# Kernel optimization log

Measured on AMD Instinct MI355X. Metric: run time of the kernel, lower is better.

Reference implementation:

```python
import jax, jax.numpy as jnp
import numpy as np
from jax import lax

EPS = 1e-5
NBITS_W = 4
NBITS_A = 4
HIDDEN = 192


def _ste(x, q):
    # straight-through estimator: forward q, backward identity
    return x + lax.stop_gradient(q - x)


def act_q(x, bit, signed):
    # ACT_Q: per-tensor uniform activation quantization with max-abs scale (STE)
    if bit >= 32:
        return x
    n = float(2 ** (bit - 1) - 1) if signed else float(2 ** bit - 1)
    scale = lax.stop_gradient(jnp.max(jnp.abs(x)) + 1e-8)
    lo = -1.0 if signed else 0.0
    xc = jnp.clip(x / scale, lo, 1.0)
    q = jnp.round(xc * n) / n * scale
    return _ste(x, q)


def weight_q(w, bit):
    # Conv2d_quan_cim weight quant: symmetric per-tensor max-abs uniform quant (STE)
    if bit >= 32:
        return w
    n = float(2 ** (bit - 1) - 1)
    scale = lax.stop_gradient(jnp.max(jnp.abs(w)) + 1e-8)
    q = jnp.round(jnp.clip(w / scale, -1.0, 1.0) * n) / n * scale
    return _ste(w, q)


def bn(x, g, b, m, v):
    # eval-mode BatchNorm2d over NCHW
    inv = lax.rsqrt(v + EPS)
    return (x - m[None, :, None, None]) * (g * inv)[None, :, None, None] + b[None, :, None, None]


def conv(x, w, stride=1, groups=1, pad=0):
    return lax.conv_general_dilated(
        x, w, (stride, stride), ((pad, pad), (pad, pad)),
        dimension_numbers=("NCHW", "OIHW", "NCHW"), feature_group_count=groups)


def setup_inputs() -> dict:
    key = jax.random.key(0)
    ks = jax.random.split(key, 16)
    f32 = jnp.float32
    return {
        "x": jax.random.normal(ks[0], (32, 32, 112, 112), dtype=f32),
        "w1": jax.random.normal(ks[1], (HIDDEN, 32, 1, 1), dtype=f32),
        "bn1_g": jax.random.uniform(ks[2], (HIDDEN,), dtype=f32),
        "bn1_b": jax.random.normal(ks[3], (HIDDEN,), dtype=f32),
        "bn1_m": jax.random.normal(ks[4], (HIDDEN,), dtype=f32),
        "bn1_v": jax.random.uniform(ks[5], (HIDDEN,), dtype=f32),
        "w_dw": jax.random.normal(ks[6], (HIDDEN, 1, 3, 3), dtype=f32),
        "bn2_g": jax.random.uniform(ks[7], (HIDDEN,), dtype=f32),
        "bn2_b": jax.random.normal(ks[8], (HIDDEN,), dtype=f32),
        "bn2_m": jax.random.normal(ks[9], (HIDDEN,), dtype=f32),
        "bn2_v": jax.random.uniform(ks[10], (HIDDEN,), dtype=f32),
        "w2": jax.random.normal(ks[11], (32, HIDDEN, 1, 1), dtype=f32),
        "bn3_g": jax.random.uniform(ks[12], (32,), dtype=f32),
        "bn3_b": jax.random.normal(ks[13], (32,), dtype=f32),
        "bn3_m": jax.random.normal(ks[14], (32,), dtype=f32),
        "bn3_v": jax.random.uniform(ks[15], (32,), dtype=f32),
    }


def reference(x, w1, bn1_g, bn1_b, bn1_m, bn1_v, w_dw, bn2_g, bn2_b, bn2_m, bn2_v,
              w2, bn3_g, bn3_b, bn3_m, bn3_v):
    # leading signed ACT_Q (first=False)
    h = act_q(x, NBITS_A, signed=True)
    # expand 1x1: Conv2d_quan_cim -> BN -> ReLU6 -> ACT_Q
    h = conv(h, weight_q(w1, NBITS_W))
    h = jnp.clip(bn(h, bn1_g, bn1_b, bn1_m, bn1_v), 0.0, 6.0)
    h = act_q(h, NBITS_A, signed=False)
    # depthwise 3x3: Conv2d_quan_cim_dw -> BN -> ReLU6 -> ACT_Q
    h = conv(h, weight_q(w_dw, NBITS_W), stride=1, groups=HIDDEN, pad=1)
    h = jnp.clip(bn(h, bn2_g, bn2_b, bn2_m, bn2_v), 0.0, 6.0)
    h = act_q(h, NBITS_A, signed=False)
    # project 1x1: Conv2d_quan_cim -> BN
    h = conv(h, weight_q(w2, NBITS_W))
    h = bn(h, bn3_g, bn3_b, bn3_m, bn3_v)
    # out_actq (signed) then residual add (use_res_connect is True here)
    h = act_q(h, NBITS_A, signed=True)
    return x + h
```

## Files before the change

### kernel.cpp

```cpp
#include <hip/hip_runtime.h>


#define HW    12544
#define WID   112
#define CIN   32
#define CMID  192
#define COUT  32
#define NB    32
#define NPIX  (NB*HW)
#define NX    (NB*CIN*HW)

#define OFF_SCAL   0
#define OFF_WSC    16
#define OFF_BN1    64
#define OFF_BN2    2368
#define OFF_BN3    4672
#define OFF_FQ1    5120
#define OFF_FQ2    7488
#define OFF_W1P    9856
#define OFF_WDW    16000
#define OFF_W1A    22912
#define OFF_W2A    29056
#define OFF_WDWT   35200
#define OFF_PMAX   42112
#define OFF_XQ     65536

typedef int v4i __attribute__((ext_vector_type(4)));
typedef unsigned long long ull;

#if defined(__has_builtin)
#if __has_builtin(__builtin_amdgcn_sdot4)
#define HAVE_SDOT4 1
#endif
#endif

__device__ __forceinline__ int sdot4(unsigned a, unsigned b, int c) {
#ifdef HAVE_SDOT4
    return __builtin_amdgcn_sdot4((int)a, (int)b, c, false);
#else
    c += (int)(signed char)(a & 0xff)        * (int)(signed char)(b & 0xff);
    c += (int)(signed char)((a >> 8) & 0xff) * (int)(signed char)((b >> 8) & 0xff);
    c += (int)(signed char)((a >> 16) & 0xff)* (int)(signed char)((b >> 16) & 0xff);
    c += (int)(signed char)(a >> 24)         * (int)(signed char)(b >> 24);
    return c;
#endif
}

__device__ __forceinline__ v4i mfma_i8(ull a, ull b, v4i c) {
    return __builtin_amdgcn_mfma_i32_16x16x32_i8((long)a, (long)b, c, 0, 0, 0);
}

__device__ __forceinline__ float bmax256(float v, float* red) {
    const int t = threadIdx.x;
    red[t] = v; __syncthreads();
    for (int s = 128; s; s >>= 1) {
        if (t < s) red[t] = fmaxf(red[t], red[t + s]);
        __syncthreads();
    }
    float r = red[0]; __syncthreads();
    return r;
}

__device__ __forceinline__ float qcode(float x, float s, float n, float lo) {
    float t = x / s;
    t = fminf(fmaxf(t, lo), 1.0f);
    return rintf(__fmul_rn(t, n));
}

__device__ __forceinline__ float bnq(float d, float C, float m, float g, float b) {
    float y = __fmul_rn(d, C);
    float h = __fadd_rn(__fmul_rn(__fsub_rn(y, m), g), b);
    return fminf(fmaxf(h, 0.f), 6.f);
}

__device__ __forceinline__ float qexact15(float h, float s) {
    return rintf(__fmul_rn(fminf(h / s, 1.f), 15.f));
}
__device__ __forceinline__ float qfast15(float df, float A, float B) {
    float t = fmaf(df, A, B);
    return rintf(fminf(fmaxf(t, 0.f), 15.f));
}

__global__ __launch_bounds__(256) void kprepx(
    const float4* __restrict__ x4,
    const float* __restrict__ w1, const float* __restrict__ wdw, const float* __restrict__ w2,
    const float* __restrict__ g1, const float* __restrict__ b1, const float* __restrict__ m1, const float* __restrict__ v1,
    const float* __restrict__ g2, const float* __restrict__ b2, const float* __restrict__ m2, const float* __restrict__ v2,
    const float* __restrict__ g3, const float* __restrict__ b3, const float* __restrict__ m3, const float* __restrict__ v3,
    unsigned char* __restrict__ ws)
{
    __shared__ float red[256];
    const int t = threadIdx.x;

    if (blockIdx.x == 0) {
        unsigned* scal = (unsigned*)(ws + OFF_SCAL);
        float* wsc  = (float*)(ws + OFF_WSC);
        float* bn1  = (float*)(ws + OFF_BN1);
        float* bn2  = (float*)(ws + OFF_BN2);
        float* bn3  = (float*)(ws + OFF_BN3);
        unsigned* w1p = (unsigned*)(ws + OFF_W1P);
        float*  wdwf  = (float*)(ws + OFF_WDW);

        if (t < 4) scal[t] = 0u;
        if (t == 0) { ((unsigned*)(ws+OFF_FQ1))[576] = 1u; ((unsigned*)(ws+OFF_FQ2))[576] = 1u; }

        float m;
        m = 0.f; for (int i = t; i < CMID*CIN; i += 256) m = fmaxf(m, fabsf(w1[i]));
        float sw1 = bmax256(m, red) + 1e-8f;
        m = 0.f; for (int i = t; i < CMID*9; i += 256) m = fmaxf(m, fabsf(wdw[i]));
        float swd = bmax256(m, red) + 1e-8f;
        m = 0.f; for (int i = t; i < COUT*CMID; i += 256) m = fmaxf(m, fabsf(w2[i]));
        float sw2 = bmax256(m, red) + 1e-8f;
        if (t == 0) { wsc[0] = sw1; wsc[1] = swd; wsc[2] = sw2; }

        for (int i = t; i < CMID*8; i += 256) {
            int oc = i >> 3, j = i & 7;
            unsigned wword = 0;
#pragma unroll
            for (int k = 0; k < 4; ++k) {
                int code = (int)qcode(w1[oc*CIN + 4*j + k], sw1, 7.f, -1.f);
                wword |= ((unsigned)code & 0xffu) << (8*k);
            }
            w1p[i] = wword;
        }
        for (int i = t; i < CMID*9; i += 256) wdwf[i] = qcode(wdw[i], swd, 7.f, -1.f);

        for (int i = t; i < 12*64; i += 256) {
            int octile = i >> 6, l = i & 63;
            int oc = octile*16 + (l & 15), icb = (l >> 4) * 8;
            unsigned lo = 0, hi = 0;
#pragma unroll
            for (int k = 0; k < 4; ++k) {
                lo |= ((unsigned)(int)qcode(w1[oc*CIN + icb + k],     sw1, 7.f, -1.f) & 0xffu) << (8*k);
                hi |= ((unsigned)(int)qcode(w1[oc*CIN + icb + 4 + k], sw1, 7.f, -1.f) & 0xffu) << (8*k);
            }
            ((unsigned*)(ws + OFF_W1A))[i*2]   = lo;
            ((unsigned*)(ws + OFF_W1A))[i*2+1] = hi;
        }
        for (int i = t; i < 2*6*64; i += 256) {
            int oct = i / 384, rem = i % 384, chunk = rem >> 6, l = rem & 63;
            int oc = oct*16 + (l & 15), cb = chunk*32 + (l >> 4) * 8;
            unsigned lo = 0, hi = 0;
#pragma unroll
            for (int k = 0; k < 4; ++k) {
                lo |= ((unsigned)(int)qcode(w2[oc*CMID + cb + k],     sw2, 7.f, -1.f) & 0xffu) << (8*k);
                hi |= ((unsigned)(int)qcode(w2[oc*CMID + cb + 4 + k], sw2, 7.f, -1.f) & 0xffu) << (8*k);
            }
            ((unsigned*)(ws + OFF_W2A))[i*2]   = lo;
            ((unsigned*)(ws + OFF_W2A))[i*2+1] = hi;
        }
        for (int i = t; i < 48*9; i += 256) {
            int qg = i / 9, tap = i % 9;
            float4 v;
            v.x = qcode(wdw[(qg*4+0)*9 + tap], swd, 7.f, -1.f);
            v.y = qcode(wdw[(qg*4+1)*9 + tap], swd, 7.f, -1.f);
            v.z = qcode(wdw[(qg*4+2)*9 + tap], swd, 7.f, -1.f);
            v.w = qcode(wdw[(qg*4+3)*9 + tap], swd, 7.f, -1.f);
            ((float4*)(ws + OFF_WDWT))[i] = v;
        }

        for (int c = t; c < CMID; c += 256) {
            float vv1 = v1[c] + 1e-5f;
            bn1[c] = __fmul_rn(g1[c], (float)(1.0 / sqrt((double)vv1)));
            bn1[192+c] = m1[c]; bn1[384+c] = b1[c];
            float vv2 = v2[c] + 1e-5f;
            bn2[c] = __fmul_rn(g2[c], (float)(1.0 / sqrt((double)vv2)));
            bn2[192+c] = m2[c]; bn2[384+c] = b2[c];
        }
        for (int c = t; c < COUT; c += 256) {
            float vv3 = v3[c] + 1e-5f;
            bn3[c] = __fmul_rn(g3[c], (float)(1.0 / sqrt((double)vv3)));
            bn3[32+c] = m3[c]; bn3[64+c] = b3[c];
        }
    }

    float m = 0.f;
    for (size_t i = (size_t)blockIdx.x*256 + t; i < NX/4; i += (size_t)gridDim.x*256) {
        float4 v = x4[i];
        m = fmaxf(m, fmaxf(fmaxf(fabsf(v.x), fabsf(v.y)), fmaxf(fabsf(v.z), fabsf(v.w))));
    }
    float r = bmax256(m, red);
    if (t == 0) ((float*)(ws + OFF_PMAX))[blockIdx.x] = r;
}

__global__ __launch_bounds__(256) void kmax1q(const float* __restrict__ x,
                                              unsigned char* __restrict__ ws)
{
    __shared__ unsigned s_w1p[CMID*8];
    __shared__ float s_bn1[576];
    __shared__ float red[256];
    const int t = threadIdx.x;

    {
        const uint4* src = (const uint4*)(ws + OFF_W1P);
        uint4* dst = (uint4*)s_w1p;
        for (int i = t; i < CMID*8/4; i += 256) dst[i] = src[i];
        const float* b = (const float*)(ws + OFF_BN1);
        for (int i = t; i < 576; i += 256) s_bn1[i] = b[i];
    }

    const float* wsc = (const float*)(ws + OFF_WSC);
    unsigned char* xq = ws + OFF_XQ;

    float pm = 0.f;
    const float* pmax = (const float*)(ws + OFF_PMAX);
    for (int i = t; i < 2048; i += 256) pm = fmaxf(pm, pmax[i]);
    float sxr = bmax256(pm, red);
    if (blockIdx.x == 0 && t == 0) ((unsigned*)(ws + OFF_SCAL))[0] = __float_as_uint(sxr);
    const float sx = sxr + 1e-8f;
    const float C1 = (float)(((double)sx / 7.0) * ((double)wsc[0] / 7.0));

    const int p = blockIdx.x * 256 + t;
    const int n = p / HW, pi = p % HW;
    const float* xp = x + (size_t)n * CIN * HW + pi;

    float kx[CIN];
#pragma unroll
    for (int ic = 0; ic < CIN; ++ic) {
        float v = xp[(size_t)ic * HW] / sx;
        v = fminf(fmaxf(v, -1.f), 1.f);
        kx[ic] = rintf(__fmul_rn(v, 7.f));
    }

    unsigned wb[8];
#pragma unroll
    for (int j = 0; j < 8; ++j) {
        unsigned b0 = (unsigned)(int)kx[4*j]     & 0xffu;
        unsigned b1 = (unsigned)(int)kx[4*j + 1] & 0xffu;
        unsigned b2 = (unsigned)(int)kx[4*j + 2] & 0xffu;
        unsigned b3 = (unsigned)(int)kx[4*j + 3] & 0xffu;
        wb[j] = b0 | (b1 << 8) | (b2 << 16) | (b3 << 24);
    }
    uint4* q4 = (uint4*)(xq + (size_t)p * 32);
    q4[0] = make_uint4(wb[0], wb[1], wb[2], wb[3]);
    q4[1] = make_uint4(wb[4], wb[5], wb[6], wb[7]);

    __syncthreads();

    float mx = 0.f;
    for (int oc = 0; oc < CMID; ++oc) {
        int d = 0;
#pragma unroll
        for (int j = 0; j < 8; ++j) d = sdot4(wb[j], s_w1p[oc*8 + j], d);
        float h = bnq((float)d, C1, s_bn1[192+oc], s_bn1[oc], s_bn1[384+oc]);
        mx = fmaxf(mx, h);
        if (__any(mx >= 6.0f)) break;
    }
    float r = bmax256(mx, red);
    if (t == 0) atomicMax((unsigned*)(ws + OFF_SCAL) + 1, __float_as_uint(r));
}

__global__ __launch_bounds__(64) void kcoef(unsigned char* __restrict__ ws, int stage)
{
    const unsigned* scal = (const unsigned*)(ws + OFF_SCAL);
    const float* wsc = (const float*)(ws + OFF_WSC);
    const int c = blockIdx.x, lane = threadIdx.x;
    const float* bn = (const float*)(ws + (stage == 1 ? OFF_BN1 : OFF_BN2));
    float* fq = (float*)(ws + (stage == 1 ? OFF_FQ1 : OFF_FQ2));

    float C, s; int R;
    if (stage == 1) {
        float sx = __uint_as_float(scal[0]) + 1e-8f;
        C = (float)(((double)sx / 7.0) * ((double)wsc[0] / 7.0));
        s = __uint_as_float(scal[1]) + 1e-8f;
        R = 1568;
    } else {
        float s1 = __uint_as_float(scal[1]) + 1e-8f;
        C = (float)(((double)s1 / 15.0) * ((double)wsc[1] / 7.0));
        s = __uint_as_float(scal[2]) + 1e-8f;
        R = 945;
    }
    const float gi = bn[c], mm = bn[192+c], bb = bn[384+c];
    const float A = (float)((double)C * (double)gi * 15.0 / (double)s);
    const float B = (float)(((double)bb - (double)mm * (double)gi) * 15.0 / (double)s);

    bool bad = false;
    for (int d = -R + lane; d <= R; d += 64) {
        float df = (float)d;
        float je = qexact15(bnq(df, C, mm, gi, bb), s);
        float jf = qfast15(df, A, B);
        if (je != jf) bad = true;
    }
    bool any = __any(bad);
    if (lane == 0) {
        unsigned flagv = any ? 0u : 1u;
        fq[c] = A; fq[192+c] = B;
        ((unsigned*)fq)[384+c] = flagv;
        atomicAnd(((unsigned*)fq) + 576, flagv);
    }
}

__global__ __launch_bounds__(256) void kmax2(unsigned char* __restrict__ ws)
{
    __shared__ unsigned s_w1p[CMID*8];
    __shared__ float s_wdw[CMID*9];
    __shared__ float s_bn2[576];
    __shared__ unsigned s_fq1[576];
    __shared__ float jl[8][256];
    __shared__ float red[256];
    __shared__ unsigned s_flag;
    const int t = threadIdx.x;

    {
        const uint4* sp = (const uint4*)(ws + OFF_W1P);
        uint4* dp = (uint4*)s_w1p;
        for (int i = t; i < CMID*8/4; i += 256) dp[i] = sp[i];
        const float* wp = (const float*)(ws + OFF_WDW);
        for (int i = t; i < CMID*9; i += 256) s_wdw[i] = wp[i];
        const float* b2p = (const float*)(ws + OFF_BN2);
        for (int i = t; i < 576; i += 256) s_bn2[i] = b2p[i];
        const unsigned* fp = (const unsigned*)(ws + OFF_FQ1);
        for (int i = t; i < 576; i += 256) s_fq1[i] = fp[i];
        if (t == 0) s_flag = 0u;
    }

    const unsigned* scal = (const unsigned*)(ws + OFF_SCAL);
    const float* wsc = (const float*)(ws + OFF_WSC);
    const float* gbn1 = (const float*)(ws + OFF_BN1);
    const unsigned char* xq = ws + OFF_XQ;

    const float sx  = __uint_as_float(scal[0]) + 1e-8f;
    const float s1v = __uint_as_float(scal[1]) + 1e-8f;
    const float C1  = (float)(((double)sx  / 7.0)  * ((double)wsc[0] / 7.0));
    const float C2  = (float)(((double)s1v / 15.0) * ((double)wsc[1] / 7.0));

    const int tile = blockIdx.x, n = blockIdx.y;
    const int ty = t >> 4, tx = t & 15;
    const int hy = (tile >> 3) * 14 - 1 + ty;
    const int wx = (tile & 7)  * 14 - 1 + tx;
    const bool inb = (hy >= 0 && hy < WID && wx >= 0 && wx < WID);
    const bool act = (ty < 14) && (tx < 14);

    unsigned wb[8];
    if (inb) {
        const uint4* q4 = (const uint4*)(xq + ((size_t)n * HW + hy * WID + wx) * 32);
        uint4 a = q4[0], b4 = q4[1];
        wb[0]=a.x; wb[1]=a.y; wb[2]=a.z; wb[3]=a.w;
        wb[4]=b4.x; wb[5]=b4.y; wb[6]=b4.z; wb[7]=b4.w;
    } else {
#pragma unroll
        for (int j = 0; j < 8; ++j) wb[j] = 0u;
    }
    __syncthreads();

    float mx = 0.f;
    for (int ph = 0; ph < CMID/8; ++ph) {
#pragma unroll
        for (int k = 0; k < 8; ++k) {
            const int c = ph*8 + k;
            int d1 = 0;
#pragma unroll
            for (int j = 0; j < 8; ++j) d1 = sdot4(wb[j], s_w1p[c*8 + j], d1);
            float j1 = 0.f;
            if (inb) {
                float d1f = (float)d1;
                if (s_fq1[384+c]) {
                    j1 = qfast15(d1f, __uint_as_float(s_fq1[c]), __uint_as_float(s_fq1[192+c]));
                } else {
                    float h1 = bnq(d1f, C1, gbn1[192+c], gbn1[c], gbn1[384+c]);
                    j1 = qexact15(h1, s1v);
                }
            }
            jl[k][t] = j1;
        }
        __syncthreads();
        if (act) {
#pragma unroll
            for (int k = 0; k < 8; ++k) {
                const int c = ph*8 + k;
                const float* wd = s_wdw + c * 9;
                float d2 = 0.f;
#pragma unroll
                for (int dy = 0; dy < 3; ++dy)
#pragma unroll
                    for (int dx = 0; dx < 3; ++dx)
                        d2 = fmaf(jl[k][(ty+dy)*16 + tx+dx], wd[dy*3+dx], d2);
                float h2 = bnq(d2, C2, s_bn2[192+c], s_bn2[c], s_bn2[384+c]);
                mx = fmaxf(mx, h2);
            }
        }
        if (mx >= 6.0f) s_flag = 1u;
        __syncthreads();
        if (s_flag) break;
    }
    float r = bmax256(mx, red);
    if (t == 0) atomicMax((unsigned*)(ws + OFF_SCAL) + 2, __float_as_uint(r));
}

__global__ __launch_bounds__(256) void kconv2(unsigned char* __restrict__ ws,
                                              float* __restrict__ h3)
{
    __shared__ ull   s_w1a[12*64];
    __shared__ ull   s_w2a[2*6*64];
    __shared__ float4 s_wdwT[48*9];
    __shared__ float s_fqA1[192], s_fqB1[192], s_fqA2[192], s_fqB2[192];
    __shared__ float s_bn1[576], s_bn2[576], s_bn3[96];
    __shared__ float4 jl4[4][256];
    __shared__ unsigned j2buf[256][8];
    __shared__ float red[256];
    __shared__ int s_af1, s_af2;
    const int t = threadIdx.x;

    {
        const uint4* a = (const uint4*)(ws + OFF_W1A);
        uint4* da = (uint4*)s_w1a;
        for (int i = t; i < 384; i += 256) da[i] = a[i];
        const uint4* b = (const uint4*)(ws + OFF_W2A);
        uint4* db = (uint4*)s_w2a;
        for (int i = t; i < 384; i += 256) db[i] = b[i];
        const uint4* c = (const uint4*)(ws + OFF_WDWT);
        uint4* dc = (uint4*)s_wdwT;
        for (int i = t; i < 432; i += 256) dc[i] = c[i];
        const float* f1 = (const float*)(ws + OFF_FQ1);
        const float* f2 = (const float*)(ws + OFF_FQ2);
        for (int i = t; i < 192; i += 256) {
            s_fqA1[i] = f1[i]; s_fqB1[i] = f1[192+i];
            s_fqA2[i] = f2[i]; s_fqB2[i] = f2[192+i];
        }
        const float* b1p = (const float*)(ws + OFF_BN1);
        const float* b2p = (const float*)(ws + OFF_BN2);
        for (int i = t; i < 576; i += 256) { s_bn1[i] = b1p[i]; s_bn2[i] = b2p[i]; }
        const float* b3p = (const float*)(ws + OFF_BN3);
        if (t < 96) s_bn3[t] = b3p[t];
        if (t == 0) {
            s_af1 = (int)((const unsigned*)(ws + OFF_FQ1))[576];
            s_af2 = (int)((const unsigned*)(ws + OFF_FQ2))[576];
        }
    }

    const unsigned* scal = (const unsigned*)(ws + OFF_SCAL);
    const float* wsc = (const float*)(ws + OFF_WSC);
    const unsigned char* xq = ws + OFF_XQ;

    const float sx  = __uint_as_float(scal[0]) + 1e-8f;
    const float s1v = __uint_as_float(scal[1]) + 1e-8f;
    const float s2v = __uint_as_float(scal[2]) + 1e-8f;
    const float C1  = (float)(((double)sx  / 7.0)  * ((double)wsc[0] / 7.0));
    const float C2  = (float)(((double)s1v / 15.0) * ((double)wsc[1] / 7.0));
    const float C3  = (float)(((double)s2v / 15.0) * ((double)wsc[2] / 7.0));

    const int tile = blockIdx.x, n = blockIdx.y;
    const int y0 = (tile >> 3) * 14, x0 = (tile & 7) * 14;
    const int lane = t & 63, wid = t >> 6;
    const int ty = t >> 4, tx = t & 15;
    const bool act = (ty < 14) && (tx < 14);
    const int px = lane & 15, kq = lane >> 4;

    ull  xb[4];
    bool okb[4];
#pragma unroll
    for (int i = 0; i < 4; ++i) {
        int g = 4*wid + i;
        int bhy = y0 - 1 + g, bwx = x0 - 1 + px;
        bool ok = (bhy >= 0) && (bhy < WID) && (bwx >= 0) && (bwx < WID);
        okb[i] = ok;
        ull v = 0;
        if (ok) v = *(const ull*)(xq + (((size_t)n * HW + bhy * WID + bwx) * 32 + kq * 8));
        xb[i] = v;
    }
    __syncthreads();

    v4i acc2[2][4];
#pragma unroll
    for (int o = 0; o < 2; ++o)
#pragma unroll
        for (int i = 0; i < 4; ++i) { acc2[o][i][0]=0; acc2[o][i][1]=0; acc2[o][i][2]=0; acc2[o][i][3]=0; }

    for (int ph = 0; ph < 12; ++ph) {
        ull a1 = s_w1a[ph*64 + lane];
        const int oc0 = ph*16 + kq*4;
        float4 A14, B14;
        A14 = *(const float4*)&s_fqA1[oc0];
        B14 = *(const float4*)&s_fqB1[oc0];
#pragma unroll
        for (int i = 0; i < 4; ++i) {
            v4i z = {0,0,0,0};
            v4i d = mfma_i8(a1, xb[i], z);
            float4 j1v;
            if (s_af1) {
                j1v.x = okb[i] ? qfast15((float)d[0], A14.x, B14.x) : 0.f;
                j1v.y = okb[i] ? qfast15((float)d[1], A14.y, B14.y) : 0.f;
                j1v.z = okb[i] ? qfast15((float)d[2], A14.z, B14.z) : 0.f;
                j1v.w = okb[i] ? qfast15((float)d[3], A14.w, B14.w) : 0.f;
            } else {
                float jj[4];
#pragma unroll
                for (int r = 0; r < 4; ++r) {
                    int oc = oc0 + r;
                    float h1 = bnq((float)d[r], C1, s_bn1[192+oc], s_bn1[oc], s_bn1[384+oc]);
                    jj[r] = okb[i] ? qexact15(h1, s1v) : 0.f;
                }
                j1v.x = jj[0]; j1v.y = jj[1]; j1v.z = jj[2]; j1v.w = jj[3];
            }
            jl4[kq][(4*wid + i)*16 + px] = j1v;
        }
        __syncthreads();

        unsigned pw0 = 0, pw1 = 0, pw2 = 0, pw3 = 0;
        if (act) {
            unsigned pw[4];
#pragma unroll
            for (int q = 0; q < 4; ++q) {
                float4 s = {0.f, 0.f, 0.f, 0.f};
#pragma unroll
                for (int dy = 0; dy < 3; ++dy)
#pragma unroll
                    for (int dx = 0; dx < 3; ++dx) {
                        float4 wv = s_wdwT[(ph*4 + q)*9 + dy*3 + dx];
                        float4 jv = jl4[q][(ty+dy)*16 + tx+dx];
                        s.x = fmaf(jv.x, wv.x, s.x);
                        s.y = fmaf(jv.y, wv.y, s.y);
                        s.z = fmaf(jv.z, wv.z, s.z);
                        s.w = fmaf(jv.w, wv.w, s.w);
                    }
                const int oc2 = ph*16 + q*4;
                float j2a, j2b, j2c, j2d;
                if (s_af2) {
                    float4 A24 = *(const float4*)&s_fqA2[oc2];
                    float4 B24 = *(const float4*)&s_fqB2[oc2];
                    j2a = qfast15(s.x, A24.x, B24.x);
                    j2b = qfast15(s.y, A24.y, B24.y);
                    j2c = qfast15(s.z, A24.z, B24.z);
                    j2d = qfast15(s.w, A24.w, B24.w);
                } else {
                    j2a = qexact15(bnq(s.x, C2, s_bn2[192+oc2],   s_bn2[oc2],   s_bn2[384+oc2]),   s2v);
                    j2b = qexact15(bnq(s.y, C2, s_bn2[192+oc2+1], s_bn2[oc2+1], s_bn2[384+oc2+1]), s2v);
                    j2c = qexact15(bnq(s.z, C2, s_bn2[192+oc2+2], s_bn2[oc2+2], s_bn2[384+oc2+2]), s2v);
                    j2d = qexact15(bnq(s.w, C2, s_bn2[192+oc2+3], s_bn2[oc2+3], s_bn2[384+oc2+3]), s2v);
                }
                pw[q] = ((unsigned)(int)j2a) | ((unsigned)(int)j2b << 8) |
                        ((unsigned)(int)j2c << 16) | ((unsigned)(int)j2d << 24);
            }
            pw0 = pw[0]; pw1 = pw[1]; pw2 = pw[2]; pw3 = pw[3];
        }
        *(uint4*)&j2buf[t][(ph & 1) * 4] = make_uint4(pw0, pw1, pw2, pw3);

        if (ph & 1) {
            __syncthreads();
            const int chunk = ph >> 1;
#pragma unroll
            for (int oct = 0; oct < 2; ++oct) {
                ull a2 = s_w2a[(oct*6 + chunk)*64 + lane];
#pragma unroll
                for (int i = 0; i < 4; ++i) {
                    int g = 4*wid + i;
                    ull b2 = *(const ull*)&j2buf[g*16 + px][kq * 2];
                    acc2[oct][i] = mfma_i8(a2, b2, acc2[oct][i]);
                }
            }
        }
        __syncthreads();
    }

    float mx = 0.f;
#pragma unroll
    for (int oct = 0; oct < 2; ++oct)
#pragma unroll
        for (int i = 0; i < 4; ++i) {
            int g = 4*wid + i;
            if (g < 14 && px < 14) {
                int gy = y0 + g, gx = x0 + px;
#pragma unroll
                for (int r = 0; r < 4; ++r) {
                    int oc = oct*16 + kq*4 + r;
                    float y = __fmul_rn((float)acc2[oct][i][r], C3);
                    float h = __fadd_rn(__fmul_rn(__fsub_rn(y, s_bn3[32+oc]), s_bn3[oc]), s_bn3[64+oc]);
                    h3[((size_t)n * COUT + oc) * HW + gy * WID + gx] = h;
                    mx = fmaxf(mx, fabsf(h));
                }
            }
        }
    float r = bmax256(mx, red);
    if (t == 0) atomicMax((unsigned*)(ws + OFF_SCAL) + 3, __float_as_uint(r));
}

__global__ __launch_bounds__(256) void kout(const float4* __restrict__ x4,
                                            float4* __restrict__ io4,
                                            const unsigned char* __restrict__ ws)
{
    const unsigned* scal = (const unsigned*)(ws + OFF_SCAL);
    const float s3v = __uint_as_float(scal[3]) + 1e-8f;

    for (size_t i = (size_t)blockIdx.x*256 + threadIdx.x; i < NX/4; i += (size_t)gridDim.x*256) {
        float4 h = io4[i], xv = x4[i], o;
        float* hp = &h.x; float* xp = &xv.x; float* op = &o.x;
#pragma unroll
        for (int k = 0; k < 4; ++k) {
            float tq = fminf(fmaxf(hp[k] / s3v, -1.f), 1.f);
            float kq = rintf(__fmul_rn(tq, 7.f));
            float q  = __fmul_rn(kq / 7.f, s3v);
            op[k] = __fadd_rn(xp[k], q);
        }
        io4[i] = o;
    }
}

extern "C" void kernel_launch(void* const* d_in, const int* in_sizes, int n_in,
                              void* d_out, int out_size, void* d_ws, size_t ws_size,
                              hipStream_t stream)
{
    const float* x   = (const float*)d_in[0];
    const float* w1  = (const float*)d_in[1];
    const float* g1  = (const float*)d_in[2];
    const float* b1  = (const float*)d_in[3];
    const float* m1  = (const float*)d_in[4];
    const float* v1  = (const float*)d_in[5];
    const float* wdw = (const float*)d_in[6];
    const float* g2  = (const float*)d_in[7];
    const float* b2  = (const float*)d_in[8];
    const float* m2  = (const float*)d_in[9];
    const float* v2  = (const float*)d_in[10];
    const float* w2  = (const float*)d_in[11];
    const float* g3  = (const float*)d_in[12];
    const float* b3  = (const float*)d_in[13];
    const float* m3  = (const float*)d_in[14];
    const float* v3  = (const float*)d_in[15];
    unsigned char* ws = (unsigned char*)d_ws;

    hipLaunchKernelGGL(kprepx, dim3(2048), dim3(256), 0, stream, (const float4*)x,
                       w1, wdw, w2, g1, b1, m1, v1, g2, b2, m2, v2, g3, b3, m3, v3, ws);
    hipLaunchKernelGGL(kmax1q, dim3(NPIX/256), dim3(256), 0, stream, x, ws);
    hipLaunchKernelGGL(kcoef, dim3(CMID), dim3(64), 0, stream, ws, 1);
    hipLaunchKernelGGL(kmax2, dim3(64, NB), dim3(256), 0, stream, ws);
    hipLaunchKernelGGL(kcoef, dim3(CMID), dim3(64), 0, stream, ws, 2);
    hipLaunchKernelGGL(kconv2, dim3(64, NB), dim3(256), 0, stream, ws, (float*)d_out);
    hipLaunchKernelGGL(kout, dim3(2048), dim3(256), 0, stream,
                       (const float4*)x, (float4*)d_out, ws);
}
```

Before: 279.3 us.

## Use packed fp16 for depthwise conv staging and pad LDS buffers

```diff
diff --git a/kernel.cpp b/kernel.cpp
--- a/kernel.cpp
+++ b/kernel.cpp
@@ -21,12 +21,22 @@
 #define OFF_WDW    16000
 #define OFF_W1A    22912
 #define OFF_W2A    29056
-#define OFF_WDWT   35200
+#define OFF_WDWH   35200
 #define OFF_PMAX   42112
 #define OFF_XQ     65536
 
+#define PADP(p) ((p) + ((p) >> 4))
+
 typedef int v4i __attribute__((ext_vector_type(4)));
 typedef unsigned long long ull;
+typedef _Float16 h2 __attribute__((ext_vector_type(2)));
+
+__device__ __forceinline__ unsigned h2u(h2 v){ union{h2 h; unsigned u;} c; c.h=v; return c.u; }
+__device__ __forceinline__ h2 u2h(unsigned u){ union{h2 h; unsigned u;} c; c.u=u; return c.h; }
+__device__ __forceinline__ h2 pkrtz(float a, float b){
+    auto r = __builtin_amdgcn_cvt_pkrtz(a, b);
+    union { decltype(r) f; h2 h; } c; c.f = r; return c.h;
+}
 
 #if defined(__has_builtin)
 #if __has_builtin(__builtin_amdgcn_sdot4)
@@ -151,12 +161,11 @@
         }
         for (int i = t; i < 48*9; i += 256) {
             int qg = i / 9, tap = i % 9;
-            float4 v;
-            v.x = qcode(wdw[(qg*4+0)*9 + tap], swd, 7.f, -1.f);
-            v.y = qcode(wdw[(qg*4+1)*9 + tap], swd, 7.f, -1.f);
-            v.z = qcode(wdw[(qg*4+2)*9 + tap], swd, 7.f, -1.f);
-            v.w = qcode(wdw[(qg*4+3)*9 + tap], swd, 7.f, -1.f);
-            ((float4*)(ws + OFF_WDWT))[i] = v;
+            float c0 = qcode(wdw[(qg*4+0)*9 + tap], swd, 7.f, -1.f);
+            float c1 = qcode(wdw[(qg*4+1)*9 + tap], swd, 7.f, -1.f);
+            float c2 = qcode(wdw[(qg*4+2)*9 + tap], swd, 7.f, -1.f);
+            float c3 = qcode(wdw[(qg*4+3)*9 + tap], swd, 7.f, -1.f);
+            ((uint2*)(ws + OFF_WDWH))[i] = make_uint2(h2u(pkrtz(c0, c1)), h2u(pkrtz(c2, c3)));
         }
 
         for (int c = t; c < CMID; c += 256) {
@@ -392,11 +401,11 @@
 {
     __shared__ ull   s_w1a[12*64];
     __shared__ ull   s_w2a[2*6*64];
-    __shared__ float4 s_wdwT[48*9];
+    __shared__ uint2 s_wdwh[48*9];
     __shared__ float s_fqA1[192], s_fqB1[192], s_fqA2[192], s_fqB2[192];
     __shared__ float s_bn1[576], s_bn2[576], s_bn3[96];
-    __shared__ float4 jl4[4][256];
-    __shared__ unsigned j2buf[256][8];
+    __shared__ uint2 jlh[4][272];
+    __shared__ unsigned j2buf[256][9];
     __shared__ float red[256];
     __shared__ int s_af1, s_af2;
     const int t = threadIdx.x;
@@ -408,9 +417,9 @@
         const uint4* b = (const uint4*)(ws + OFF_W2A);
         uint4* db = (uint4*)s_w2a;
         for (int i = t; i < 384; i += 256) db[i] = b[i];
-        const uint4* c = (const uint4*)(ws + OFF_WDWT);
-        uint4* dc = (uint4*)s_wdwT;
-        for (int i = t; i < 432; i += 256) dc[i] = c[i];
+        const uint4* c = (const uint4*)(ws + OFF_WDWH);
+        uint4* dc = (uint4*)s_wdwh;
+        for (int i = t; i < 216; i += 256) dc[i] = c[i];
         const float* f1 = (const float*)(ws + OFF_FQ1);
         const float* f2 = (const float*)(ws + OFF_FQ2);
         for (int i = t; i < 192; i += 256) {
@@ -469,9 +478,8 @@
     for (int ph = 0; ph < 12; ++ph) {
         ull a1 = s_w1a[ph*64 + lane];
         const int oc0 = ph*16 + kq*4;
-        float4 A14, B14;
-        A14 = *(const float4*)&s_fqA1[oc0];
-        B14 = *(const float4*)&s_fqB1[oc0];
+        float4 A14 = *(const float4*)&s_fqA1[oc0];
+        float4 B14 = *(const float4*)&s_fqB1[oc0];
 #pragma unroll
         for (int i = 0; i < 4; ++i) {
             v4i z = {0,0,0,0};
@@ -492,64 +500,66 @@
                 }
                 j1v.x = jj[0]; j1v.y = jj[1]; j1v.z = jj[2]; j1v.w = jj[3];
             }
-            jl4[kq][(4*wid + i)*16 + px] = j1v;
+            jlh[kq][PADP((4*wid + i)*16 + px)] =
+                make_uint2(h2u(pkrtz(j1v.x, j1v.y)), h2u(pkrtz(j1v.z, j1v.w)));
         }
         __syncthreads();
 
-        unsigned pw0 = 0, pw1 = 0, pw2 = 0, pw3 = 0;
+        unsigned pw[4] = {0u, 0u, 0u, 0u};
         if (act) {
-            unsigned pw[4];
 #pragma unroll
             for (int q = 0; q < 4; ++q) {
-                float4 s = {0.f, 0.f, 0.f, 0.f};
+                h2 s01 = u2h(0u), s23 = u2h(0u);
+                const int qg = ph*4 + q;
 #pragma unroll
                 for (int dy = 0; dy < 3; ++dy)
 #pragma unroll
                     for (int dx = 0; dx < 3; ++dx) {
-                        float4 wv = s_wdwT[(ph*4 + q)*9 + dy*3 + dx];
-                        float4 jv = jl4[q][(ty+dy)*16 + tx+dx];
-                        s.x = fmaf(jv.x, wv.x, s.x);
-                        s.y = fmaf(jv.y, wv.y, s.y);
-                        s.z = fmaf(jv.z, wv.z, s.z);
-                        s.w = fmaf(jv.w, wv.w, s.w);
+                        uint2 jv = jlh[q][PADP((ty+dy)*16 + tx+dx) - ((ty+dy)*16 + tx+dx == 0 ? 0 : 0)];
+                        jv = jlh[q][PADP((ty+dy)*16 + (tx+dx))];
+                        uint2 wv = s_wdwh[qg*9 + dy*3 + dx];
+                        s01 += u2h(jv.x) * u2h(wv.x);
+                        s23 += u2h(jv.y) * u2h(wv.y);
                     }
+                float f0 = (float)s01[0], f1 = (float)s01[1];
+                float f2 = (float)s23[0], f3 = (float)s23[1];
                 const int oc2 = ph*16 + q*4;
                 float j2a, j2b, j2c, j2d;
                 if (s_af2) {
                     float4 A24 = *(const float4*)&s_fqA2[oc2];
                     float4 B24 = *(const float4*)&s_fqB2[oc2];
-                    j2a = qfast15(s.x, A24.x, B24.x);
-                    j2b = qfast15(s.y, A24.y, B24.y);
-                    j2c = qfast15(s.z, A24.z, B24.z);
-                    j2d = qfast15(s.w, A24.w, B24.w);
+                    j2a = qfast15(f0, A24.x, B24.x);
+                    j2b = qfast15(f1, A24.y, B24.y);
+                    j2c = qfast15(f2, A24.z, B24.z);
+                    j2d = qfast15(f3, A24.w, B24.w);
                 } else {
-                    j2a = qexact15(bnq(s.x, C2, s_bn2[192+oc2],   s_bn2[oc2],   s_bn2[384+oc2]),   s2v);
-                    j2b = qexact15(bnq(s.y, C2, s_bn2[192+oc2+1], s_bn2[oc2+1], s_bn2[384+oc2+1]), s2v);
-                    j2c = qexact15(bnq(s.z, C2, s_bn2[192+oc2+2], s_bn2[oc2+2], s_bn2[384+oc2+2]), s2v);
-                    j2d = qexact15(bnq(s.w, C2, s_bn2[192+oc2+3], s_bn2[oc2+3], s_bn2[384+oc2+3]), s2v);
+                    j2a = qexact15(bnq(f0, C2, s_bn2[192+oc2],   s_bn2[oc2],   s_bn2[384+oc2]),   s2v);
+                    j2b = qexact15(bnq(f1, C2, s_bn2[192+oc2+1], s_bn2[oc2+1], s_bn2[384+oc2+1]), s2v);
+                    j2c = qexact15(bnq(f2, C2, s_bn2[192+oc2+2], s_bn2[oc2+2], s_bn2[384+oc2+2]), s2v);
+                    j2d = qexact15(bnq(f3, C2, s_bn2[192+oc2+3], s_bn2[oc2+3], s_bn2[384+oc2+3]), s2v);
                 }
                 pw[q] = ((unsigned)(int)j2a) | ((unsigned)(int)j2b << 8) |
                         ((unsigned)(int)j2c << 16) | ((unsigned)(int)j2d << 24);
             }
-            pw0 = pw[0]; pw1 = pw[1]; pw2 = pw[2]; pw3 = pw[3];
-        }
-        *(uint4*)&j2buf[t][(ph & 1) * 4] = make_uint4(pw0, pw1, pw2, pw3);
+        }
+#pragma unroll
+        for (int q = 0; q < 4; ++q) j2buf[t][(ph & 1) * 4 + q] = pw[q];
+        __syncthreads();
 
         if (ph & 1) {
-            __syncthreads();
             const int chunk = ph >> 1;
 #pragma unroll
             for (int oct = 0; oct < 2; ++oct) {
                 ull a2 = s_w2a[(oct*6 + chunk)*64 + lane];
 #pragma unroll
                 for (int i = 0; i < 4; ++i) {
-                    int g = 4*wid + i;
-                    ull b2 = *(const ull*)&j2buf[g*16 + px][kq * 2];
+                    int row = (4*wid + i)*16 + px;
+                    unsigned w0 = j2buf[row][kq*2], w1 = j2buf[row][kq*2 + 1];
+                    ull b2 = (ull)w0 | ((ull)w1 << 32);
                     acc2[oct][i] = mfma_i8(a2, b2, acc2[oct][i]);
                 }
             }
         }
-        __syncthreads();
     }
 
     float mx = 0.f;
```

Result: faster. 257.2 us (-7.9%).
